# Performance work log

Hardware: AMD Instinct MI355X
Metric: run time of the kernel (lower is better)

The kernel has to match this reference:

```python
import jax, jax.numpy as jnp
import numpy as np

N_NODES = 50000
N_EDGES = 800000
D_IN = 128
D_OUT = 128


def setup_inputs() -> dict:
    key = jax.random.key(0)
    k1, k2, k3, k4, k5 = jax.random.split(key, 5)
    x = jax.random.normal(k1, (N_NODES, D_IN), dtype=jnp.float32)
    edge_index = jax.random.randint(k2, (2, N_EDGES), 0, N_NODES, dtype=jnp.int64)
    scale = 1.0 / np.sqrt(D_IN)
    W_rel = jax.random.normal(k3, (D_OUT, D_IN), dtype=jnp.float32) * scale
    b_rel = jax.random.normal(k4, (D_OUT,), dtype=jnp.float32) * scale
    W_root = jax.random.normal(k5, (D_OUT, D_IN), dtype=jnp.float32) * scale
    return {"x": x, "edge_index": edge_index, "W_rel": W_rel, "b_rel": b_rel, "W_root": W_root}


def reference(x, edge_index, W_rel, b_rel, W_root):
    # PyG GraphConv (aggr='add'):
    #   out_i = W_rel @ (sum_{j->i} x_j) + b_rel + W_root @ x_i
    # followed by ReLU (normalization=None, dropout=0 -> identity).
    src = edge_index[0]  # message source j
    dst = edge_index[1]  # message target i
    n = x.shape[0]
    agg = jax.ops.segment_sum(x[src], dst, num_segments=n)  # [N, D_IN]
    out = agg @ W_rel.T + b_rel + x @ W_root.T              # [N, D_OUT]
    return jax.nn.relu(out)
```

## Files before the change

kernel.cpp:

```cpp
#include <hip/hip_runtime.h>
#include <hip/hip_bf16.h>


#define N_NODES 50000
#define N_EDGES 800000
#define D 128
#define SLOTS 40
#define NB 782
#define BCAP 1536
#define BINB 196
#define NPB 32
#define KC 32
#define SROW 136

#define CVT_N  (N_NODES * (D / 2))
#define PACK_N (8 * 8 * 64 * 8)

typedef __attribute__((ext_vector_type(8))) short short8;
typedef __attribute__((ext_vector_type(4))) float floatx4;

__device__ __forceinline__ float bf2f(unsigned short u) {
    return __uint_as_float((unsigned int)u << 16);
}
__device__ __forceinline__ unsigned short f2bf(float f) {
    __hip_bfloat16 h = __float2bfloat16(f);
    return *(unsigned short*)&h;
}

__device__ __forceinline__ int wave_detect_i64(const int* __restrict__ ei) {
    int lane = threadIdx.x & 63;
    int v = ei[2 * lane + 1];
    return __ballot(v == 0) == ~0ull;
}

__global__ __launch_bounds__(256) void zero_f4_kernel(float4* __restrict__ p, int n4) {
    int i = blockIdx.x * 256 + threadIdx.x;
    if (i < n4) p[i] = make_float4(0.f, 0.f, 0.f, 0.f);
}

__global__ void detect_kernel(const int* __restrict__ ei, int* __restrict__ flag) {
    if (threadIdx.x == 0 && blockIdx.x == 0) {
        int any = 0;
        for (int i = 0; i < 64; ++i) any |= ei[2 * i + 1];
        flag[0] = (any == 0) ? 1 : 0;
    }
}

__global__ __launch_bounds__(256) void stage1_kernel(const float2* __restrict__ x2,
                                                     ushort2* __restrict__ xb2,
                                                     const float* __restrict__ Wrel,
                                                     const float* __restrict__ Wroot,
                                                     unsigned short* __restrict__ pwc,
                                                     const int* __restrict__ ei,
                                                     int* __restrict__ gcur,
                                                     unsigned* __restrict__ bmem,
                                                     int* __restrict__ ovf_cnt,
                                                     int* __restrict__ ovf) {
    __shared__ int lds_cnt[NB];
    __shared__ int lds_base[NB];
    if (blockIdx.x < BINB) {
        int t = threadIdx.x;
        int i64 = wave_detect_i64(ei);
        for (int i = t; i < NB; i += 256) lds_cnt[i] = 0;
        __syncthreads();

        unsigned rec[16];
        int rnk[16];
#pragma unroll
        for (int g = 0; g < 4; ++g) {
            int base = blockIdx.x * 4096 + g * 1024 + t * 4;
            int s0 = -1, s1 = -1, s2 = -1, s3 = -1;
            int d0 = -1, d1 = -1, d2 = -1, d3 = -1;
            if (base < N_EDGES) {
                if (i64) {
                    int4 a = *(const int4*)&ei[2 * base];
                    int4 b = *(const int4*)&ei[2 * base + 4];
                    s0 = a.x; s1 = a.z; s2 = b.x; s3 = b.z;
                    int4 c = *(const int4*)&ei[2 * N_EDGES + 2 * base];
                    int4 e = *(const int4*)&ei[2 * N_EDGES + 2 * base + 4];
                    d0 = c.x; d1 = c.z; d2 = e.x; d3 = e.z;
                } else {
                    int4 sv = *(const int4*)&ei[base];
                    int4 dv = *(const int4*)&ei[N_EDGES + base];
                    s0 = sv.x; s1 = sv.y; s2 = sv.z; s3 = sv.w;
                    d0 = dv.x; d1 = dv.y; d2 = dv.z; d3 = dv.w;
                }
            }
#define BINP(idx, ss, dd)                                                        \
            {                                                                    \
                bool ok = (unsigned)(ss) < N_NODES && (unsigned)(dd) < N_NODES;  \
                rec[idx] = ok ? (((unsigned)(dd) << 16) | (unsigned)(ss))        \
                              : 0xFFFFFFFFu;                                     \
                rnk[idx] = ok ? atomicAdd(&lds_cnt[(unsigned)(dd) >> 6], 1) : 0; \
            }
            BINP(g * 4 + 0, s0, d0)
            BINP(g * 4 + 1, s1, d1)
            BINP(g * 4 + 2, s2, d2)
            BINP(g * 4 + 3, s3, d3)
#undef BINP
        }
        __syncthreads();
        for (int i = t; i < NB; i += 256) {
            int c = lds_cnt[i];
            lds_base[i] = c ? atomicAdd(&gcur[i], c) : 0;
        }
        __syncthreads();
#pragma unroll
        for (int idx = 0; idx < 16; ++idx) {
            unsigned r = rec[idx];
            if (r != 0xFFFFFFFFu) {
                int bk = (int)(r >> 22);
                int pos = lds_base[bk] + rnk[idx];
                if (pos < BCAP) {
                    bmem[(size_t)bk * BCAP + pos] = r;
                } else {
                    int o = atomicAdd(ovf_cnt, 1);
                    ovf[2 * o] = (int)(r >> 16);
                    ovf[2 * o + 1] = (int)(r & 0xFFFFu);
                }
            }
        }
    } else {
        int i = (blockIdx.x - BINB) * 256 + threadIdx.x;
        if (i < CVT_N) {
            float2 f = x2[i];
            xb2[i] = make_ushort2(f2bf(f.x), f2bf(f.y));
        } else if (i < CVT_N + PACK_N) {
            int idx  = i - CVT_N;
            int j    = idx & 7;
            int lane = (idx >> 3) & 63;
            int n0   = (idx >> 9) & 7;
            int t    = idx >> 12;
            int n = n0 * 16 + (lane & 15);
            int k = t * 32 + (lane >> 4) * 8 + j;
            float w = (k < D) ? Wrel[n * D + k] : Wroot[n * D + (k - D)];
            pwc[idx] = f2bf(w);
        }
    }
}

__global__ __launch_bounds__(256) void stage2_kernel(const int* __restrict__ gcur,
                                                     const unsigned* __restrict__ bmem,
                                                     int* __restrict__ cnt,
                                                     unsigned short* __restrict__ slots,
                                                     int* __restrict__ ovf_cnt,
                                                     int* __restrict__ ovf) {
    __shared__ int lc[64];
    int b = blockIdx.x, t = threadIdx.x;
    if (t < 64) lc[t] = 0;
    __syncthreads();
    int n = gcur[b];
    if (n > BCAP) n = BCAP;
    for (int e = t; e < n; e += 256) {
        unsigned r = bmem[(size_t)b * BCAP + e];
        int d = (int)(r >> 16);
        int s = (int)(r & 0xFFFFu);
        int p = atomicAdd(&lc[d & 63], 1);
        if (p < SLOTS) {
            slots[d * SLOTS + p] = (unsigned short)s;
        } else {
            int o = atomicAdd(ovf_cnt, 1);
            ovf[2 * o] = d;
            ovf[2 * o + 1] = s;
        }
    }
    __syncthreads();
    if (t < 64) {
        int node = b * 64 + t;
        if (node < N_NODES) cnt[node] = lc[t];
    }
}

__global__ __launch_bounds__(256) void GraphConvLayer_55783035240593_kernel(
        const ushort2* __restrict__ xb2,
        const unsigned short* __restrict__ xb,
        const int* __restrict__ cnt,
        const unsigned short* __restrict__ slots,
        const int* __restrict__ ovf_cnt,
        const int* __restrict__ ovf,
        const unsigned short* __restrict__ pwc,
        const float* __restrict__ b_rel,
        float* __restrict__ out) {
    __shared__ unsigned short sA[16 * SROW];
    int wid  = threadIdx.x >> 6;
    int lane = threadIdx.x & 63;
    int node0 = blockIdx.x * 16;
    int tov = ovf_cnt[0];

    for (int li = 0; li < 4; ++li) {
        int node = node0 + wid * 4 + li;
        int kk = cnt[node];
        if (kk > SLOTS) kk = SLOTS;
        int myidx = (lane < kk) ? (int)slots[node * SLOTS + lane] : 0;
        float ax = 0.f, ay = 0.f;
        for (int j = 0; j < kk; j += 8) {
            int s0 = __shfl(myidx, j);
            int s1 = __shfl(myidx, j + 1);
            int s2 = __shfl(myidx, j + 2);
            int s3 = __shfl(myidx, j + 3);
            int s4 = __shfl(myidx, j + 4);
            int s5 = __shfl(myidx, j + 5);
            int s6 = __shfl(myidx, j + 6);
            int s7 = __shfl(myidx, j + 7);
            ushort2 u0 = xb2[(size_t)s0 * (D / 2) + lane];
            ushort2 u1 = xb2[(size_t)s1 * (D / 2) + lane];
            ushort2 u2 = xb2[(size_t)s2 * (D / 2) + lane];
            ushort2 u3 = xb2[(size_t)s3 * (D / 2) + lane];
            ushort2 u4 = xb2[(size_t)s4 * (D / 2) + lane];
            ushort2 u5 = xb2[(size_t)s5 * (D / 2) + lane];
            ushort2 u6 = xb2[(size_t)s6 * (D / 2) + lane];
            ushort2 u7 = xb2[(size_t)s7 * (D / 2) + lane];
            float m1 = (j + 1 < kk) ? 1.f : 0.f;
            float m2 = (j + 2 < kk) ? 1.f : 0.f;
            float m3 = (j + 3 < kk) ? 1.f : 0.f;
            float m4 = (j + 4 < kk) ? 1.f : 0.f;
            float m5 = (j + 5 < kk) ? 1.f : 0.f;
            float m6 = (j + 6 < kk) ? 1.f : 0.f;
            float m7 = (j + 7 < kk) ? 1.f : 0.f;
            ax += bf2f(u0.x) + m1 * bf2f(u1.x) + m2 * bf2f(u2.x) + m3 * bf2f(u3.x)
                + m4 * bf2f(u4.x) + m5 * bf2f(u5.x) + m6 * bf2f(u6.x) + m7 * bf2f(u7.x);
            ay += bf2f(u0.y) + m1 * bf2f(u1.y) + m2 * bf2f(u2.y) + m3 * bf2f(u3.y)
                + m4 * bf2f(u4.y) + m5 * bf2f(u5.y) + m6 * bf2f(u6.y) + m7 * bf2f(u7.y);
        }
        if (tov > 0) {
            for (int t2 = 0; t2 < tov; ++t2) {
                if (ovf[2 * t2] == node) {
                    ushort2 u = xb2[(size_t)ovf[2 * t2 + 1] * (D / 2) + lane];
                    ax += bf2f(u.x);
                    ay += bf2f(u.y);
                }
            }
        }
        *(ushort2*)&sA[(wid * 4 + li) * SROW + 2 * lane] =
            make_ushort2(f2bf(ax), f2bf(ay));
    }
    __syncthreads();

    int m = lane & 15, quad = lane >> 4;
    const unsigned short* arow = &sA[m * SROW + quad * 8];
    const unsigned short* xrow = xb + (size_t)(node0 + m) * D + quad * 8;

    floatx4 acc0 = (floatx4){0.f, 0.f, 0.f, 0.f};
    floatx4 acc1 = (floatx4){0.f, 0.f, 0.f, 0.f};
#pragma unroll
    for (int t = 0; t < 8; ++t) {
        short8 afrag = (t < 4) ? *(const short8*)(arow + t * 32)
                               : *(const short8*)(xrow + (t - 4) * 32);
        const unsigned short* bb = pwc + ((size_t)(t * 8 + wid * 2) * 64 + lane) * 8;
        short8 b0 = *(const short8*)bb;
        short8 b1 = *(const short8*)(bb + 64 * 8);
        acc0 = __builtin_amdgcn_mfma_f32_16x16x32_bf16(afrag, b0, acc0, 0, 0, 0);
        acc1 = __builtin_amdgcn_mfma_f32_16x16x32_bf16(afrag, b1, acc1, 0, 0, 0);
    }

#pragma unroll
    for (int q = 0; q < 2; ++q) {
        floatx4 a = q ? acc1 : acc0;
        int n = (wid * 2 + q) * 16 + m;
        float bias = b_rel[n];
#pragma unroll
        for (int r = 0; r < 4; ++r) {
            int node = node0 + quad * 4 + r;
            out[(size_t)node * D + n] = fmaxf(a[r] + bias, 0.f);
        }
    }
}

__global__ __launch_bounds__(256) void pack_w_kernel(const float* __restrict__ W,
                                                     float* __restrict__ pw) {
    int idx = blockIdx.x * 256 + threadIdx.x;
    if (idx >= D * D) return;
    int o = idx >> 7, k = idx & 127;
    pw[k * D + o] = W[o * D + k];
}

__global__ __launch_bounds__(256) void hist_kernel(const int* __restrict__ ei,
                                                   int* __restrict__ deg) {
    int i64 = wave_detect_i64(ei);
    int base = (blockIdx.x * 256 + threadIdx.x) * 4;
    if (base >= N_EDGES) return;
    int d0, d1, d2, d3;
    if (i64) {
        int4 a = *(const int4*)&ei[2 * N_EDGES + 2 * base];
        int4 b = *(const int4*)&ei[2 * N_EDGES + 2 * base + 4];
        d0 = a.x; d1 = a.z; d2 = b.x; d3 = b.z;
    } else {
        int4 v = *(const int4*)&ei[N_EDGES + base];
        d0 = v.x; d1 = v.y; d2 = v.z; d3 = v.w;
    }
    if ((unsigned)d0 < N_NODES) atomicAdd(&deg[d0], 1);
    if ((unsigned)d1 < N_NODES) atomicAdd(&deg[d1], 1);
    if ((unsigned)d2 < N_NODES) atomicAdd(&deg[d2], 1);
    if ((unsigned)d3 < N_NODES) atomicAdd(&deg[d3], 1);
}

__device__ __forceinline__ int wave_iscan(int v, int lane) {
#pragma unroll
    for (int off = 1; off < 64; off <<= 1) {
        int u = __shfl_up(v, off, 64);
        if (lane >= off) v += u;
    }
    return v;
}

__global__ __launch_bounds__(1024) void scan_kernel(const int* __restrict__ deg,
                                                    int* __restrict__ offsets,
                                                    int* __restrict__ cursor) {
    __shared__ int wsum[16];
    __shared__ int base_s;
    int t = threadIdx.x, lane = t & 63, w = t >> 6;
    if (t == 0) { base_s = 0; offsets[0] = 0; }
    __syncthreads();
    for (int c0 = 0; c0 < N_NODES; c0 += 1024) {
        int idx = c0 + t;
        int v = (idx < N_NODES) ? deg[idx] : 0;
        int inc = wave_iscan(v, lane);
        if (lane == 63) wsum[w] = inc;
        __syncthreads();
        if (w == 0) {
            int s = (lane < 16) ? wsum[lane] : 0;
            int si = wave_iscan(s, lane);
            if (lane < 16) wsum[lane] = si - s;
        }
        __syncthreads();
        int tot = base_s + wsum[w] + inc;
        if (idx < N_NODES) {
            offsets[idx + 1] = tot;
            cursor[idx] = tot - v;
        }
        __syncthreads();
        if (t == 1023) base_s = tot;
        __syncthreads();
    }
}

__global__ __launch_bounds__(256) void reorder_kernel(const int* __restrict__ ei,
                                                      int* __restrict__ cursor,
                                                      int* __restrict__ csr_src) {
    int i64 = wave_detect_i64(ei);
    int base = (blockIdx.x * 256 + threadIdx.x) * 4;
    if (base >= N_EDGES) return;
    int s0, s1, s2, s3, d0, d1, d2, d3;
    if (i64) {
        int4 a = *(const int4*)&ei[2 * base];
        int4 b = *(const int4*)&ei[2 * base + 4];
        s0 = a.x; s1 = a.z; s2 = b.x; s3 = b.z;
        int4 c = *(const int4*)&ei[2 * N_EDGES + 2 * base];
        int4 e = *(const int4*)&ei[2 * N_EDGES + 2 * base + 4];
        d0 = c.x; d1 = c.z; d2 = e.x; d3 = e.z;
    } else {
        int4 sv = *(const int4*)&ei[base];
        int4 dv = *(const int4*)&ei[N_EDGES + base];
        s0 = sv.x; s1 = sv.y; s2 = sv.z; s3 = sv.w;
        d0 = dv.x; d1 = dv.y; d2 = dv.z; d3 = dv.w;
    }
    bool v0 = (unsigned)s0 < N_NODES && (unsigned)d0 < N_NODES;
    bool v1 = (unsigned)s1 < N_NODES && (unsigned)d1 < N_NODES;
    bool v2 = (unsigned)s2 < N_NODES && (unsigned)d2 < N_NODES;
    bool v3 = (unsigned)s3 < N_NODES && (unsigned)d3 < N_NODES;
    int p0 = v0 ? atomicAdd(&cursor[d0], 1) : 0;
    int p1 = v1 ? atomicAdd(&cursor[d1], 1) : 0;
    int p2 = v2 ? atomicAdd(&cursor[d2], 1) : 0;
    int p3 = v3 ? atomicAdd(&cursor[d3], 1) : 0;
    if (v0) csr_src[p0] = s0;
    if (v1) csr_src[p1] = s1;
    if (v2) csr_src[p2] = s2;
    if (v3) csr_src[p3] = s3;
}

__global__ __launch_bounds__(256) void gather_kernel(const float2* __restrict__ x2,
                                                     const int* __restrict__ csr_src,
                                                     const int* __restrict__ offsets,
                                                     float2* __restrict__ agg2) {
    int node = blockIdx.x * 4 + (threadIdx.x >> 6);
    int lane = threadIdx.x & 63;
    if (node >= N_NODES) return;
    int beg = offsets[node], end = offsets[node + 1];
    float2 acc = make_float2(0.f, 0.f);
    for (int e = beg; e < end; ++e) {
        int s = csr_src[e];
        float2 f = x2[(size_t)s * (D / 2) + lane];
        acc.x += f.x;
        acc.y += f.y;
    }
    agg2[(size_t)node * (D / 2) + lane] = acc;
}

__global__ __launch_bounds__(256) void scatter_kernel(const float2* __restrict__ x2,
                                                      const int* __restrict__ ei,
                                                      const int* __restrict__ flag,
                                                      float* __restrict__ agg) {
    int wave = threadIdx.x >> 6;
    int lane = threadIdx.x & 63;
    int e = blockIdx.x * 4 + wave;
    if (e >= N_EDGES) return;
    int i64 = flag ? flag[0] : 0;
    int s, d;
    if (i64) { s = ei[2 * e]; d = ei[2 * N_EDGES + 2 * e]; }
    else     { s = ei[e];     d = ei[N_EDGES + e]; }
    if ((unsigned)s >= N_NODES || (unsigned)d >= N_NODES) return;
    float2 f = x2[(size_t)s * (D / 2) + lane];
    atomicAdd(&agg[(size_t)d * D + 2 * lane + 0], f.x);
    atomicAdd(&agg[(size_t)d * D + 2 * lane + 1], f.y);
}

__global__ __launch_bounds__(256) void gemm_f32_kernel(
        const float2* __restrict__ x2,
        const float* __restrict__ pwrel,
        const float* __restrict__ pwroot,
        const float* __restrict__ b_rel,
        float* __restrict__ out) {
    __shared__ float sWrel[KC * D];
    __shared__ float sWroot[KC * D];
    __shared__ float2 sAm[NPB * (KC / 2)];
    __shared__ float2 sXm[NPB * (KC / 2)];

    int t = threadIdx.x;
    int node0 = blockIdx.x * NPB;
    int tn = t >> 5;
    int to = t & 31;

    float acc[4][4];
#pragma unroll
    for (int a = 0; a < 4; ++a)
#pragma unroll
        for (int b = 0; b < 4; ++b) acc[a][b] = 0.0f;

    for (int c = 0; c < 4; ++c) {
        __syncthreads();
#pragma unroll
        for (int r = 0; r < 4; ++r) {
            int i = r * 256 + t;
            ((float4*)sWrel)[i]  = ((const float4*)(pwrel  + c * KC * D))[i];
            ((float4*)sWroot)[i] = ((const float4*)(pwroot + c * KC * D))[i];
        }
#pragma unroll
        for (int r = 0; r < 2; ++r) {
            int i = r * 256 + t;
            int n = i >> 4, k2 = i & 15;
            int node = node0 + n;
            float2 av = make_float2(0.f, 0.f), xv = make_float2(0.f, 0.f);
            if (node < N_NODES) {
                av = ((const float2*)out)[(size_t)node * (D / 2) + c * (KC / 2) + k2];
                xv = x2[(size_t)node * (D / 2) + c * (KC / 2) + k2];
            }
            sAm[i] = av;
            sXm[i] = xv;
        }
        __syncthreads();

#pragma unroll
        for (int k2 = 0; k2 < KC / 2; ++k2) {
            float4 wr0 = *(const float4*)&sWrel[(2 * k2 + 0) * D + to * 4];
            float4 wr1 = *(const float4*)&sWrel[(2 * k2 + 1) * D + to * 4];
            float4 wt0 = *(const float4*)&sWroot[(2 * k2 + 0) * D + to * 4];
            float4 wt1 = *(const float4*)&sWroot[(2 * k2 + 1) * D + to * 4];
#pragma unroll
            for (int ni = 0; ni < 4; ++ni) {
                float2 a  = sAm[(tn * 4 + ni) * (KC / 2) + k2];
                float2 xx = sXm[(tn * 4 + ni) * (KC / 2) + k2];
                acc[ni][0] += a.x * wr0.x + a.y * wr1.x + xx.x * wt0.x + xx.y * wt1.x;
                acc[ni][1] += a.x * wr0.y + a.y * wr1.y + xx.x * wt0.y + xx.y * wt1.y;
                acc[ni][2] += a.x * wr0.z + a.y * wr1.z + xx.x * wt0.z + xx.y * wt1.z;
                acc[ni][3] += a.x * wr0.w + a.y * wr1.w + xx.x * wt0.w + xx.y * wt1.w;
            }
        }
    }

    int o0 = to * 4;
    float4 bias = *(const float4*)&b_rel[o0];
#pragma unroll
    for (int ni = 0; ni < 4; ++ni) {
        int node = node0 + tn * 4 + ni;
        if (node >= N_NODES) continue;
        float4 v;
        v.x = fmaxf(acc[ni][0] + bias.x, 0.f);
        v.y = fmaxf(acc[ni][1] + bias.y, 0.f);
        v.z = fmaxf(acc[ni][2] + bias.z, 0.f);
        v.w = fmaxf(acc[ni][3] + bias.w, 0.f);
        *(float4*)&out[(size_t)node * D + o0] = v;
    }
}

__global__ __launch_bounds__(128) void gemm_fallback_kernel(const float* __restrict__ x,
                                                            const float* __restrict__ Wrel,
                                                            const float* __restrict__ Wroot,
                                                            const float* __restrict__ b_rel,
                                                            float* __restrict__ out) {
    __shared__ float rowA[D];
    __shared__ float rowX[D];
    int node = blockIdx.x;
    int o = threadIdx.x;
    rowA[o] = out[(size_t)node * D + o];
    rowX[o] = x[(size_t)node * D + o];
    __syncthreads();
    float acc = b_rel[o];
    const float4* wr = (const float4*)&Wrel[o * D];
    const float4* wt = (const float4*)&Wroot[o * D];
#pragma unroll 8
    for (int k4 = 0; k4 < D / 4; ++k4) {
        float4 w = wr[k4], u = wt[k4];
        const float* a = &rowA[k4 * 4];
        const float* xx = &rowX[k4 * 4];
        acc += a[0] * w.x + a[1] * w.y + a[2] * w.z + a[3] * w.w
             + xx[0] * u.x + xx[1] * u.y + xx[2] * u.z + xx[3] * u.w;
    }
    __syncthreads();
    out[(size_t)node * D + o] = fmaxf(acc, 0.f);
}

extern "C" void kernel_launch(void* const* d_in, const int* in_sizes, int n_in,
                              void* d_out, int out_size, void* d_ws, size_t ws_size,
                              hipStream_t stream) {
    const float* x      = (const float*)d_in[0];
    const int*   ei     = (const int*)d_in[1];
    const float* W_rel  = (const float*)d_in[2];
    const float* b_rel  = (const float*)d_in[3];
    const float* W_root = (const float*)d_in[4];
    float*       out    = (float*)d_out;

    char* p = (char*)d_ws;
    size_t o0 = 16;
    int*            flag    = (int*)p;
    unsigned short* pwc     = (unsigned short*)(p + o0);  o0 += (size_t)PACK_N * 2;
    unsigned short* xb      = (unsigned short*)(p + o0);  o0 += (size_t)N_NODES * D * 2;
    int*            cnt     = (int*)(p + o0);             o0 += (size_t)N_NODES * 4;
    const size_t gcur_pad = ((size_t)NB * 4 + 15) & ~(size_t)15;
    int*            gcur    = (int*)(p + o0);             o0 += gcur_pad;
    int*            ovf_cnt = (int*)(p + o0);             o0 += 16;
    unsigned short* slots   = (unsigned short*)(p + o0);  o0 += (size_t)N_NODES * SLOTS * 2;
    unsigned*       bmem    = (unsigned*)(p + o0);        o0 += (size_t)NB * BCAP * 4;
    int*            ovf     = (int*)(p + o0);             o0 += (size_t)N_EDGES * 8;
    const size_t need_full = o0;

    size_t m0 = 16;
    float* m_pwrel  = (float*)(p + m0);  m0 += (size_t)D * D * 4;
    float* m_pwroot = (float*)(p + m0);  m0 += (size_t)D * D * 4;
    int*   m_deg    = (int*)(p + m0);    m0 += (size_t)N_NODES * 4;
    int*   m_offs   = (int*)(p + m0);    m0 += ((size_t)N_NODES + 1) * 4 + 12;
    m0 &= ~15ull;
    int*   m_csr    = (int*)(p + m0);    m0 += (size_t)N_EDGES * 4;
    const size_t need_mid = m0;
    const size_t need_pw  = 16 + 2 * (size_t)D * D * 4;

    const int eb4 = (N_EDGES / 4 + 255) / 256;

    if (ws_size >= need_full) {
        hipMemsetAsync(gcur, 0, gcur_pad + 16, stream);
        const int prep_total = CVT_N + PACK_N;
        const int grid1 = BINB + (prep_total + 255) / 256;
        stage1_kernel<<<grid1, 256, 0, stream>>>(
            (const float2*)x, (ushort2*)xb, W_rel, W_root, pwc, ei,
            gcur, bmem, ovf_cnt, ovf);
        stage2_kernel<<<NB, 256, 0, stream>>>(gcur, bmem, cnt, slots, ovf_cnt, ovf);
        GraphConvLayer_55783035240593_kernel<<<N_NODES / 16, 256, 0, stream>>>(
            (const ushort2*)xb, xb, cnt, slots, ovf_cnt, ovf, pwc, b_rel, out);
    } else if (ws_size >= need_mid) {
        pack_w_kernel<<<64, 256, 0, stream>>>(W_rel, m_pwrel);
        pack_w_kernel<<<64, 256, 0, stream>>>(W_root, m_pwroot);
        zero_f4_kernel<<<(N_NODES / 4 + 255) / 256, 256, 0, stream>>>((float4*)m_deg,
                                                                      N_NODES / 4);
        hist_kernel<<<eb4, 256, 0, stream>>>(ei, m_deg);
        scan_kernel<<<1, 1024, 0, stream>>>(m_deg, m_offs, m_deg);
        reorder_kernel<<<eb4, 256, 0, stream>>>(ei, m_deg, m_csr);
        gather_kernel<<<N_NODES / 4, 256, 0, stream>>>((const float2*)x, m_csr,
                                                       m_offs, (float2*)out);
        gemm_f32_kernel<<<(N_NODES + NPB - 1) / NPB, 256, 0, stream>>>(
            (const float2*)x, m_pwrel, m_pwroot, b_rel, out);
    } else {
        bool have_flag = ws_size >= 16;
        bool have_pw   = ws_size >= need_pw;
        if (have_flag) detect_kernel<<<1, 64, 0, stream>>>(ei, flag);
        if (have_pw) {
            pack_w_kernel<<<64, 256, 0, stream>>>(W_rel, m_pwrel);
            pack_w_kernel<<<64, 256, 0, stream>>>(W_root, m_pwroot);
        }
        int n4 = N_NODES * D / 4;
        zero_f4_kernel<<<(n4 + 255) / 256, 256, 0, stream>>>((float4*)out, n4);
        scatter_kernel<<<N_EDGES / 4, 256, 0, stream>>>((const float2*)x, ei,
                                                        have_flag ? flag : nullptr, out);
        if (have_pw)
            gemm_f32_kernel<<<(N_NODES + NPB - 1) / NPB, 256, 0, stream>>>(
                (const float2*)x, m_pwrel, m_pwroot, b_rel, out);
        else
            gemm_fallback_kernel<<<N_NODES, 128, 0, stream>>>(x, W_rel, W_root, b_rel, out);
    }
}
```

Before: 148.7 us.

## Fuse bucket-to-slot scatter into the main aggregation/GEMM kernel

Removes the separate stage2 kernel. Each block of the main kernel now reads its half of a 64-node bucket from bmem and builds per-node slot lists in shared memory, so the global slots/cnt arrays and one launch go away. Blocks now cover 32 nodes, each wave gathers two nodes at once to keep more loads in flight, and each wave computes four MFMA column tiles instead of two. Nodes that overflow their slot capacity fall back to rescanning the whole bucket. Each bucket is also read twice, once by each of its two blocks.

```diff
diff --git a/kernel.cpp b/kernel.cpp
--- a/kernel.cpp
+++ b/kernel.cpp
@@ -139,129 +139,154 @@
     }
 }
 
-__global__ __launch_bounds__(256) void stage2_kernel(const int* __restrict__ gcur,
-                                                     const unsigned* __restrict__ bmem,
-                                                     int* __restrict__ cnt,
-                                                     unsigned short* __restrict__ slots,
-                                                     int* __restrict__ ovf_cnt,
-                                                     int* __restrict__ ovf) {
-    __shared__ int lc[64];
-    int b = blockIdx.x, t = threadIdx.x;
-    if (t < 64) lc[t] = 0;
-    __syncthreads();
-    int n = gcur[b];
-    if (n > BCAP) n = BCAP;
-    for (int e = t; e < n; e += 256) {
-        unsigned r = bmem[(size_t)b * BCAP + e];
-        int d = (int)(r >> 16);
-        int s = (int)(r & 0xFFFFu);
-        int p = atomicAdd(&lc[d & 63], 1);
-        if (p < SLOTS) {
-            slots[d * SLOTS + p] = (unsigned short)s;
-        } else {
-            int o = atomicAdd(ovf_cnt, 1);
-            ovf[2 * o] = d;
-            ovf[2 * o + 1] = s;
-        }
-    }
-    __syncthreads();
-    if (t < 64) {
-        int node = b * 64 + t;
-        if (node < N_NODES) cnt[node] = lc[t];
-    }
-}
-
 __global__ __launch_bounds__(256) void GraphConvLayer_55783035240593_kernel(
         const ushort2* __restrict__ xb2,
         const unsigned short* __restrict__ xb,
-        const int* __restrict__ cnt,
-        const unsigned short* __restrict__ slots,
+        const int* __restrict__ gcur,
+        const unsigned* __restrict__ bmem,
         const int* __restrict__ ovf_cnt,
         const int* __restrict__ ovf,
         const unsigned short* __restrict__ pwc,
         const float* __restrict__ b_rel,
         float* __restrict__ out) {
-    __shared__ unsigned short sA[16 * SROW];
-    int wid  = threadIdx.x >> 6;
-    int lane = threadIdx.x & 63;
-    int node0 = blockIdx.x * 16;
+    __shared__ unsigned short sA[32 * SROW];
+    __shared__ unsigned short slotsL[32 * SLOTS];
+    __shared__ int lc[32];
+    int t = threadIdx.x;
+    int wid = t >> 6, lane = t & 63;
+    int bkt = blockIdx.x >> 1, half = blockIdx.x & 1;
+    int node0 = blockIdx.x * 32;
+
+    if (t < 32) lc[t] = 0;
+    __syncthreads();
+
+    int n = gcur[bkt];
+    if (n > BCAP) n = BCAP;
+    for (int e = t; e < n; e += 256) {
+        unsigned r = bmem[(size_t)bkt * BCAP + e];
+        int d = (int)(r >> 16);
+        if (((d >> 5) & 1) != half) continue;
+        int p = atomicAdd(&lc[d & 31], 1);
+        if (p < SLOTS) slotsL[(d & 31) * SLOTS + p] = (unsigned short)(r & 0xFFFFu);
+    }
+    __syncthreads();
     int tov = ovf_cnt[0];
 
-    for (int li = 0; li < 4; ++li) {
-        int node = node0 + wid * 4 + li;
-        int kk = cnt[node];
-        if (kk > SLOTS) kk = SLOTS;
-        int myidx = (lane < kk) ? (int)slots[node * SLOTS + lane] : 0;
-        float ax = 0.f, ay = 0.f;
-        for (int j = 0; j < kk; j += 8) {
-            int s0 = __shfl(myidx, j);
-            int s1 = __shfl(myidx, j + 1);
-            int s2 = __shfl(myidx, j + 2);
-            int s3 = __shfl(myidx, j + 3);
-            int s4 = __shfl(myidx, j + 4);
-            int s5 = __shfl(myidx, j + 5);
-            int s6 = __shfl(myidx, j + 6);
-            int s7 = __shfl(myidx, j + 7);
-            ushort2 u0 = xb2[(size_t)s0 * (D / 2) + lane];
-            ushort2 u1 = xb2[(size_t)s1 * (D / 2) + lane];
-            ushort2 u2 = xb2[(size_t)s2 * (D / 2) + lane];
-            ushort2 u3 = xb2[(size_t)s3 * (D / 2) + lane];
-            ushort2 u4 = xb2[(size_t)s4 * (D / 2) + lane];
-            ushort2 u5 = xb2[(size_t)s5 * (D / 2) + lane];
-            ushort2 u6 = xb2[(size_t)s6 * (D / 2) + lane];
-            ushort2 u7 = xb2[(size_t)s7 * (D / 2) + lane];
-            float m1 = (j + 1 < kk) ? 1.f : 0.f;
-            float m2 = (j + 2 < kk) ? 1.f : 0.f;
-            float m3 = (j + 3 < kk) ? 1.f : 0.f;
-            float m4 = (j + 4 < kk) ? 1.f : 0.f;
-            float m5 = (j + 5 < kk) ? 1.f : 0.f;
-            float m6 = (j + 6 < kk) ? 1.f : 0.f;
-            float m7 = (j + 7 < kk) ? 1.f : 0.f;
-            ax += bf2f(u0.x) + m1 * bf2f(u1.x) + m2 * bf2f(u2.x) + m3 * bf2f(u3.x)
-                + m4 * bf2f(u4.x) + m5 * bf2f(u5.x) + m6 * bf2f(u6.x) + m7 * bf2f(u7.x);
-            ay += bf2f(u0.y) + m1 * bf2f(u1.y) + m2 * bf2f(u2.y) + m3 * bf2f(u3.y)
-                + m4 * bf2f(u4.y) + m5 * bf2f(u5.y) + m6 * bf2f(u6.y) + m7 * bf2f(u7.y);
+    for (int pp = 0; pp < 4; ++pp) {
+        int la = wid * 8 + pp * 2, lb = la + 1;
+        int nodeA = node0 + la, nodeB = node0 + lb;
+        int kkA = lc[la], kkB = lc[lb];
+        int kA = (kkA > SLOTS) ? 0 : kkA;
+        int kB = (kkB > SLOTS) ? 0 : kkB;
+        int myA = (lane < kA) ? (int)slotsL[la * SLOTS + lane] : 0;
+        int myB = (lane < kB) ? (int)slotsL[lb * SLOTS + lane] : 0;
+        float axA = 0.f, ayA = 0.f, axB = 0.f, ayB = 0.f;
+        int jmax = kA > kB ? kA : kB;
+        for (int j = 0; j < jmax; j += 8) {
+            bool doA = j < kA, doB = j < kB;
+            ushort2 u[8], v[8];
+            if (doA) {
+                int s[8];
+#pragma unroll
+                for (int i = 0; i < 8; ++i) s[i] = __shfl(myA, j + i);
+#pragma unroll
+                for (int i = 0; i < 8; ++i) u[i] = xb2[(size_t)s[i] * (D / 2) + lane];
+            }
+            if (doB) {
+                int s[8];
+#pragma unroll
+                for (int i = 0; i < 8; ++i) s[i] = __shfl(myB, j + i);
+#pragma unroll
+                for (int i = 0; i < 8; ++i) v[i] = xb2[(size_t)s[i] * (D / 2) + lane];
+            }
+            if (doA) {
+#pragma unroll
+                for (int i = 0; i < 8; ++i) {
+                    float mm = (j + i < kA) ? 1.f : 0.f;
+                    axA += mm * bf2f(u[i].x);
+                    ayA += mm * bf2f(u[i].y);
+                }
+            }
+            if (doB) {
+#pragma unroll
+                for (int i = 0; i < 8; ++i) {
+                    float mm = (j + i < kB) ? 1.f : 0.f;
+                    axB += mm * bf2f(v[i].x);
+                    ayB += mm * bf2f(v[i].y);
+                }
+            }
+        }
+        if (kkA > SLOTS) {
+            for (int e = 0; e < n; ++e) {
+                unsigned r = bmem[(size_t)bkt * BCAP + e];
+                if ((int)(r >> 16) == nodeA) {
+                    ushort2 uu = xb2[(size_t)(r & 0xFFFFu) * (D / 2) + lane];
+                    axA += bf2f(uu.x); ayA += bf2f(uu.y);
+                }
+            }
+        }
+        if (kkB > SLOTS) {
+            for (int e = 0; e < n; ++e) {
+                unsigned r = bmem[(size_t)bkt * BCAP + e];
+                if ((int)(r >> 16) == nodeB) {
+                    ushort2 uu = xb2[(size_t)(r & 0xFFFFu) * (D / 2) + lane];
+                    axB += bf2f(uu.x); ayB += bf2f(uu.y);
+                }
+            }
         }
         if (tov > 0) {
-            for (int t2 = 0; t2 < tov; ++t2) {
-                if (ovf[2 * t2] == node) {
-                    ushort2 u = xb2[(size_t)ovf[2 * t2 + 1] * (D / 2) + lane];
-                    ax += bf2f(u.x);
-                    ay += bf2f(u.y);
+            for (int e2 = 0; e2 < tov; ++e2) {
+                int dd = ovf[2 * e2];
+                if (dd == nodeA) {
+                    ushort2 uu = xb2[(size_t)ovf[2 * e2 + 1] * (D / 2) + lane];
+                    axA += bf2f(uu.x); ayA += bf2f(uu.y);
+                } else if (dd == nodeB) {
+                    ushort2 uu = xb2[(size_t)ovf[2 * e2 + 1] * (D / 2) + lane];
+                    axB += bf2f(uu.x); ayB += bf2f(uu.y);
                 }
             }
         }
-        *(ushort2*)&sA[(wid * 4 + li) * SROW + 2 * lane] =
-            make_ushort2(f2bf(ax), f2bf(ay));
+        *(ushort2*)&sA[la * SROW + 2 * lane] = make_ushort2(f2bf(axA), f2bf(ayA));
+        *(ushort2*)&sA[lb * SROW + 2 * lane] = make_ushort2(f2bf(axB), f2bf(ayB));
     }
     __syncthreads();
 
     int m = lane & 15, quad = lane >> 4;
-    const unsigned short* arow = &sA[m * SROW + quad * 8];
-    const unsigned short* xrow = xb + (size_t)(node0 + m) * D + quad * 8;
+    int tl = wid >> 1, ng0 = (wid & 1) * 4;
+    const unsigned short* arow = &sA[(tl * 16 + m) * SROW + quad * 8];
+    int xnode = node0 + tl * 16 + m;
+    if (xnode >= N_NODES) xnode = 0;
+    const unsigned short* xrow = xb + (size_t)xnode * D + quad * 8;
 
     floatx4 acc0 = (floatx4){0.f, 0.f, 0.f, 0.f};
     floatx4 acc1 = (floatx4){0.f, 0.f, 0.f, 0.f};
-#pragma unroll
-    for (int t = 0; t < 8; ++t) {
-        short8 afrag = (t < 4) ? *(const short8*)(arow + t * 32)
-                               : *(const short8*)(xrow + (t - 4) * 32);
-        const unsigned short* bb = pwc + ((size_t)(t * 8 + wid * 2) * 64 + lane) * 8;
+    floatx4 acc2 = (floatx4){0.f, 0.f, 0.f, 0.f};
+    floatx4 acc3 = (floatx4){0.f, 0.f, 0.f, 0.f};
+#pragma unroll
+    for (int tt = 0; tt < 8; ++tt) {
+        short8 afrag = (tt < 4) ? *(const short8*)(arow + tt * 32)
+                                : *(const short8*)(xrow + (tt - 4) * 32);
+        const unsigned short* bb = pwc + ((size_t)(tt * 8 + ng0) * 64 + lane) * 8;
         short8 b0 = *(const short8*)bb;
-        short8 b1 = *(const short8*)(bb + 64 * 8);
+        short8 b1 = *(const short8*)(bb + 1 * 64 * 8);
+        short8 b2 = *(const short8*)(bb + 2 * 64 * 8);
+        short8 b3 = *(const short8*)(bb + 3 * 64 * 8);
         acc0 = __builtin_amdgcn_mfma_f32_16x16x32_bf16(afrag, b0, acc0, 0, 0, 0);
         acc1 = __builtin_amdgcn_mfma_f32_16x16x32_bf16(afrag, b1, acc1, 0, 0, 0);
-    }
-
-#pragma unroll
-    for (int q = 0; q < 2; ++q) {
-        floatx4 a = q ? acc1 : acc0;
-        int n = (wid * 2 + q) * 16 + m;
-        float bias = b_rel[n];
+        acc2 = __builtin_amdgcn_mfma_f32_16x16x32_bf16(afrag, b2, acc2, 0, 0, 0);
+        acc3 = __builtin_amdgcn_mfma_f32_16x16x32_bf16(afrag, b3, acc3, 0, 0, 0);
+    }
+
+#pragma unroll
+    for (int q = 0; q < 4; ++q) {
+        floatx4 a = (q == 0) ? acc0 : (q == 1) ? acc1 : (q == 2) ? acc2 : acc3;
+        int nn = (ng0 + q) * 16 + m;
+        float bias = b_rel[nn];
 #pragma unroll
         for (int r = 0; r < 4; ++r) {
-            int node = node0 + quad * 4 + r;
-            out[(size_t)node * D + n] = fmaxf(a[r] + bias, 0.f);
+            int node = node0 + tl * 16 + quad * 4 + r;
+            if (node < N_NODES)
+                out[(size_t)node * D + nn] = fmaxf(a[r] + bias, 0.f);
         }
     }
 }
@@ -524,11 +549,9 @@
     int*            flag    = (int*)p;
     unsigned short* pwc     = (unsigned short*)(p + o0);  o0 += (size_t)PACK_N * 2;
     unsigned short* xb      = (unsigned short*)(p + o0);  o0 += (size_t)N_NODES * D * 2;
-    int*            cnt     = (int*)(p + o0);             o0 += (size_t)N_NODES * 4;
     const size_t gcur_pad = ((size_t)NB * 4 + 15) & ~(size_t)15;
     int*            gcur    = (int*)(p + o0);             o0 += gcur_pad;
     int*            ovf_cnt = (int*)(p + o0);             o0 += 16;
-    unsigned short* slots   = (unsigned short*)(p + o0);  o0 += (size_t)N_NODES * SLOTS * 2;
     unsigned*       bmem    = (unsigned*)(p + o0);        o0 += (size_t)NB * BCAP * 4;
     int*            ovf     = (int*)(p + o0);             o0 += (size_t)N_EDGES * 8;
     const size_t need_full = o0;
@@ -552,9 +575,8 @@
         stage1_kernel<<<grid1, 256, 0, stream>>>(
             (const float2*)x, (ushort2*)xb, W_rel, W_root, pwc, ei,
             gcur, bmem, ovf_cnt, ovf);
-        stage2_kernel<<<NB, 256, 0, stream>>>(gcur, bmem, cnt, slots, ovf_cnt, ovf);
-        GraphConvLayer_55783035240593_kernel<<<N_NODES / 16, 256, 0, stream>>>(
-            (const ushort2*)xb, xb, cnt, slots, ovf_cnt, ovf, pwc, b_rel, out);
+        GraphConvLayer_55783035240593_kernel<<<2 * NB, 256, 0, stream>>>(
+            (const ushort2*)xb, xb, gcur, bmem, ovf_cnt, ovf, pwc, b_rel, out);
     } else if (ws_size >= need_mid) {
         pack_w_kernel<<<64, 256, 0, stream>>>(W_rel, m_pwrel);
         pack_w_kernel<<<64, 256, 0, stream>>>(W_root, m_pwroot);
```

Measured after the change: 151.6 us. About the same (+2.0%).
